# Performance work log

Hardware: AMD Instinct MI355X
Metric: run time of the kernel (lower is better)

The kernel has to match this reference:

```python
import jax, jax.numpy as jnp
import numpy as np

E = 8      # number of parts/experts
H = 128    # hidden width
D_IN = 3   # xyz coords
D_OUT = 1  # occupancy


def setup_inputs() -> dict:
    key = jax.random.key(0)
    ks = jax.random.split(key, 9)
    coords = jax.random.normal(ks[0], (1, 65536, D_IN), dtype=jnp.float32)
    s = 0.05
    return {
        "coords": coords,
        "W0": jax.random.normal(ks[1], (E, H, D_IN), dtype=jnp.float32) * s,
        "b0": jax.random.normal(ks[2], (E, H), dtype=jnp.float32) * s,
        "W1": jax.random.normal(ks[3], (E, H, H), dtype=jnp.float32) * s,
        "b1": jax.random.normal(ks[4], (E, H), dtype=jnp.float32) * s,
        "W2": jax.random.normal(ks[5], (E, H, H), dtype=jnp.float32) * s,
        "b2": jax.random.normal(ks[6], (E, H), dtype=jnp.float32) * s,
        "Wo": jax.random.normal(ks[7], (E, D_OUT, H), dtype=jnp.float32) * s,
        "bo": jax.random.normal(ks[8], (E, D_OUT), dtype=jnp.float32) * s,
    }


def reference(coords, W0, b0, W1, b1, W2, b2, Wo, bo):
    # Batched (grouped) MLP over experts: equivalent to vmap(functional_call)
    # over stacked per-part parameters in the torch module.
    # coords: [B, N, 3]; weights: [E, out, in]
    h = jax.nn.relu(jnp.einsum('bnd,ehd->ebnh', coords, W0) + b0[:, None, None, :])
    h = jax.nn.relu(jnp.einsum('ebnh,egh->ebng', h, W1) + b1[:, None, None, :])
    h = jax.nn.relu(jnp.einsum('ebnh,egh->ebng', h, W2) + b2[:, None, None, :])
    expert_out = jnp.einsum('ebnh,eoh->ebno', h, Wo) + bo[:, None, None, :]  # [E,B,N,1]
    max_occ = jnp.max(expert_out, axis=0)  # combine experts via max, [B,N,1]
    return max_occ
```

## Files before the change

kernel.cpp:

```cpp
#include <hip/hip_runtime.h>

#define NE 8
#define HD 128
#define NPTS 65536
#define TM 64

typedef __bf16 bf16x8 __attribute__((ext_vector_type(8)));
typedef __bf16 bf16x4 __attribute__((ext_vector_type(4)));
typedef float f32x4 __attribute__((ext_vector_type(4)));

__device__ __forceinline__ unsigned int f2bf(float f) {
    unsigned int u = __float_as_uint(f);
    u += 0x7FFFu + ((u >> 16) & 1u);
    return u >> 16;
}

__device__ __forceinline__ unsigned int swz(int row, int byte_in_row) {
    return (unsigned int)((row * 256 + byte_in_row) ^ ((row & 7) << 4));
}

__device__ __forceinline__ void bar_lds() {
    asm volatile("s_waitcnt lgkmcnt(0)\ns_barrier" ::: "memory");
}

template<int KB0, int KB1>
__device__ __forceinline__ void loadA128(const unsigned short* __restrict__ Ag,
                                         bf16x8 (&a)[2][4], int tc, int lr, int lg) {
#pragma unroll
    for (int ca = 0; ca < 2; ++ca)
#pragma unroll
        for (int kb = KB0; kb < KB1; ++kb)
            a[ca][kb] = *(const bf16x8*)(Ag + (tc + ca * 16 + lr) * HD + kb * 32 + lg * 8);
}

__device__ __forceinline__ void loadA32(const unsigned short* __restrict__ Ag,
                                        bf16x8 (&a)[2][1], int tc, int lr, int lg) {
#pragma unroll
    for (int ca = 0; ca < 2; ++ca)
        a[ca][0] = *(const bf16x8*)(Ag + (tc + ca * 16 + lr) * 32 + lg * 8);
}

template<int NKB, bool BSWZ, int BSTR>
__device__ __forceinline__ void gemm_core(const bf16x8 (&a)[2][NKB], const char* Bb,
                                          f32x4 (&acc)[2][4], int lr, int lg) {
#pragma unroll
    for (int kb = 0; kb < NKB; ++kb) {
        bf16x8 b[4];
#pragma unroll
        for (int nb = 0; nb < 4; ++nb) {
            int r = nb * 16 + lr;
            int byte = kb * 64 + lg * 16;
            const char* p = BSWZ ? (Bb + swz(r, byte)) : (Bb + r * BSTR + byte);
            b[nb] = *(const bf16x8*)p;
        }
#pragma unroll
        for (int ca = 0; ca < 2; ++ca)
#pragma unroll
            for (int nb = 0; nb < 4; ++nb)
                acc[ca][nb] = __builtin_amdgcn_mfma_f32_16x16x32_bf16(a[ca][kb], b[nb], acc[ca][nb], 0, 0, 0);
    }
}

__device__ __forceinline__ void epi_store(const f32x4 (&acc)[2][4], char* Db,
                                          const float* __restrict__ bias,
                                          int tc, int lr, int lg) {
#pragma unroll
    for (int ca = 0; ca < 2; ++ca) {
        int c0 = tc + ca * 16 + lg * 4;
        float4 bs = *(const float4*)(bias + c0);
#pragma unroll
        for (int nb = 0; nb < 4; ++nb) {
            int r = nb * 16 + lr;
            bf16x4 pk;
            pk[0] = (__bf16)fmaxf(acc[ca][nb][0] + bs.x, 0.f);
            pk[1] = (__bf16)fmaxf(acc[ca][nb][1] + bs.y, 0.f);
            pk[2] = (__bf16)fmaxf(acc[ca][nb][2] + bs.z, 0.f);
            pk[3] = (__bf16)fmaxf(acc[ca][nb][3] + bs.w, 0.f);
            *(bf16x4*)(Db + swz(r, c0 * 2)) = pk;
        }
    }
}

__global__ void prep_kernel(const float* __restrict__ W0,
                            const float* __restrict__ W1,
                            const float* __restrict__ W2,
                            unsigned int* __restrict__ W1b,
                            unsigned int* __restrict__ W2b,
                            unsigned int* __restrict__ W0p) {
    int i = blockIdx.x * 256 + threadIdx.x;
    float2 v = *(const float2*)(W1 + 2 * i);
    W1b[i] = f2bf(v.x) | (f2bf(v.y) << 16);
    float2 u = *(const float2*)(W2 + 2 * i);
    W2b[i] = f2bf(u.x) | (f2bf(u.y) << 16);
    if (i < NE * HD * 16) {
        int row = i >> 4;
        int kk = (i & 15) * 2;
        float a = (kk < 3) ? W0[row * 3 + kk] : 0.f;
        float b = (kk + 1 < 3) ? W0[row * 3 + kk + 1] : 0.f;
        W0p[i] = f2bf(a) | (f2bf(b) << 16);
    }
}

__global__ __launch_bounds__(256, 4) void moe_main(
    const float* __restrict__ coords,
    const float* __restrict__ b0, const float* __restrict__ b1,
    const float* __restrict__ b2,
    const float* __restrict__ Wo, const float* __restrict__ bo,
    const unsigned short* __restrict__ W0p,
    const unsigned short* __restrict__ W1b,
    const unsigned short* __restrict__ W2b,
    float* __restrict__ out) {
    __shared__ __align__(16) unsigned short hA[TM * HD];
    __shared__ __align__(16) unsigned short hB[TM * HD];
    __shared__ __align__(16) unsigned short Xp[TM * 32];
    __shared__ __align__(16) float part[256];

    const int tid = threadIdx.x;
    const int lane = tid & 63;
    const int w = tid >> 6;
    const int lr = lane & 15;
    const int lg = lane >> 4;
    const int tc = w * 32;
    const int row0 = blockIdx.x * TM;

    for (int i = tid; i < TM * 32; i += 256) Xp[i] = 0;
    __syncthreads();
    if (tid < TM * 3) {
        int r = tid / 3, k = tid % 3;
        Xp[r * 32 + k] = (unsigned short)f2bf(coords[row0 * 3 + tid]);
    }
    __syncthreads();

    float bmax = -3.0e38f;
    bf16x8 a0[2][1], a1[2][4], a2[2][4];
    loadA32(W0p, a0, tc, lr, lg);

    for (int e = 0; e < NE; ++e) {
        const unsigned short* W1e = W1b + e * HD * HD;
        const unsigned short* W2e = W2b + e * HD * HD;

        loadA128<0, 2>(W1e, a1, tc, lr, lg);
        f32x4 acc[2][4];
#pragma unroll
        for (int ca = 0; ca < 2; ++ca)
#pragma unroll
            for (int nb = 0; nb < 4; ++nb) acc[ca][nb] = (f32x4){0.f, 0.f, 0.f, 0.f};
        gemm_core<1, false, 64>(a0, (const char*)Xp, acc, lr, lg);
        epi_store(acc, (char*)hA, b0 + e * HD, tc, lr, lg);
        bar_lds();

        loadA128<2, 4>(W1e, a1, tc, lr, lg);
        loadA128<0, 2>(W2e, a2, tc, lr, lg);
#pragma unroll
        for (int ca = 0; ca < 2; ++ca)
#pragma unroll
            for (int nb = 0; nb < 4; ++nb) acc[ca][nb] = (f32x4){0.f, 0.f, 0.f, 0.f};
        gemm_core<4, true, 0>(a1, (const char*)hA, acc, lr, lg);
        epi_store(acc, (char*)hB, b1 + e * HD, tc, lr, lg);
        bar_lds();

        loadA128<2, 4>(W2e, a2, tc, lr, lg);
        loadA32(W0p + (e < 7 ? e + 1 : 7) * HD * 32, a0, tc, lr, lg);
#pragma unroll
        for (int ca = 0; ca < 2; ++ca)
#pragma unroll
            for (int nb = 0; nb < 4; ++nb) acc[ca][nb] = (f32x4){0.f, 0.f, 0.f, 0.f};
        gemm_core<4, true, 0>(a2, (const char*)hB, acc, lr, lg);

        {
            const float* b2e = b2 + e * HD;
            const float* Woe = Wo + e * HD;
            float s[4] = {0.f, 0.f, 0.f, 0.f};
#pragma unroll
            for (int ca = 0; ca < 2; ++ca) {
                int c0 = tc + ca * 16 + lg * 4;
                float4 bs = *(const float4*)(b2e + c0);
                float4 wo = *(const float4*)(Woe + c0);
#pragma unroll
                for (int nb = 0; nb < 4; ++nb) {
                    float v0 = fmaxf(acc[ca][nb][0] + bs.x, 0.f);
                    float v1 = fmaxf(acc[ca][nb][1] + bs.y, 0.f);
                    float v2 = fmaxf(acc[ca][nb][2] + bs.z, 0.f);
                    float v3 = fmaxf(acc[ca][nb][3] + bs.w, 0.f);
                    s[nb] += v0 * wo.x + v1 * wo.y + v2 * wo.z + v3 * wo.w;
                }
            }
#pragma unroll
            for (int nb = 0; nb < 4; ++nb) {
                s[nb] += __shfl_xor(s[nb], 16);
                s[nb] += __shfl_xor(s[nb], 32);
            }
            if (lg == 0) {
#pragma unroll
                for (int nb = 0; nb < 4; ++nb) part[w * 64 + nb * 16 + lr] = s[nb];
            }
        }
        bar_lds();

        if (tid < TM) {
            float v = part[tid] + part[64 + tid] + part[128 + tid] + part[192 + tid] + bo[e];
            bmax = fmaxf(bmax, v);
        }
    }

    if (tid < TM) out[row0 + tid] = bmax;
}

extern "C" void kernel_launch(void* const* d_in, const int* in_sizes, int n_in,
                              void* d_out, int out_size, void* d_ws, size_t ws_size,
                              hipStream_t stream) {
    const float* coords = (const float*)d_in[0];
    const float* W0 = (const float*)d_in[1];
    const float* b0 = (const float*)d_in[2];
    const float* W1 = (const float*)d_in[3];
    const float* b1 = (const float*)d_in[4];
    const float* W2 = (const float*)d_in[5];
    const float* b2 = (const float*)d_in[6];
    const float* Wo = (const float*)d_in[7];
    const float* bo = (const float*)d_in[8];
    float* out = (float*)d_out;

    char* ws = (char*)d_ws;
    unsigned short* W1b = (unsigned short*)(ws);
    unsigned short* W2b = (unsigned short*)(ws + 262144);
    unsigned short* W0p = (unsigned short*)(ws + 524288);

    prep_kernel<<<dim3(256), dim3(256), 0, stream>>>(
        W0, W1, W2, (unsigned int*)W1b, (unsigned int*)W2b, (unsigned int*)W0p);

    moe_main<<<dim3(NPTS / TM), dim3(256), 0, stream>>>(
        coords, b0, b1, b2, Wo, bo, W0p, W1b, W2b, out);
}
```

Measured before the change: 78.35 us.

## Retile waves as 2x2 over hidden channels and points, prefetch next expert weights

Each wave now covers 64 hidden channels by 32 points instead of 32 channels by all 64 points. This halves the number of LDS B-operand reads per MFMA, and the reduction partials drop from four per point to two. Weight loads are moved so the next expert's W0 and first half of W1 are prefetched during the last GEMM and its epilogue, to hide global latency. The X tile row stride is padded to 40 to reduce bank conflicts. The cost is roughly double the per-wave weight register footprint (a1/a2 grow to 4x4 vectors), which may hurt occupancy under launch_bounds(256,4) or cause spills.

```diff
diff --git a/kernel.cpp b/kernel.cpp
--- a/kernel.cpp
+++ b/kernel.cpp
@@ -24,53 +24,32 @@
 }
 
 template<int KB0, int KB1>
-__device__ __forceinline__ void loadA128(const unsigned short* __restrict__ Ag,
-                                         bf16x8 (&a)[2][4], int tc, int lr, int lg) {
-#pragma unroll
-    for (int ca = 0; ca < 2; ++ca)
+__device__ __forceinline__ void loadW(const unsigned short* __restrict__ Ag,
+                                      bf16x8 (&a)[4][4], int tc, int lr, int lg) {
+#pragma unroll
+    for (int ca = 0; ca < 4; ++ca)
 #pragma unroll
         for (int kb = KB0; kb < KB1; ++kb)
             a[ca][kb] = *(const bf16x8*)(Ag + (tc + ca * 16 + lr) * HD + kb * 32 + lg * 8);
 }
 
-__device__ __forceinline__ void loadA32(const unsigned short* __restrict__ Ag,
-                                        bf16x8 (&a)[2][1], int tc, int lr, int lg) {
-#pragma unroll
-    for (int ca = 0; ca < 2; ++ca)
-        a[ca][0] = *(const bf16x8*)(Ag + (tc + ca * 16 + lr) * 32 + lg * 8);
-}
-
-template<int NKB, bool BSWZ, int BSTR>
-__device__ __forceinline__ void gemm_core(const bf16x8 (&a)[2][NKB], const char* Bb,
-                                          f32x4 (&acc)[2][4], int lr, int lg) {
-#pragma unroll
-    for (int kb = 0; kb < NKB; ++kb) {
-        bf16x8 b[4];
-#pragma unroll
-        for (int nb = 0; nb < 4; ++nb) {
-            int r = nb * 16 + lr;
-            int byte = kb * 64 + lg * 16;
-            const char* p = BSWZ ? (Bb + swz(r, byte)) : (Bb + r * BSTR + byte);
-            b[nb] = *(const bf16x8*)p;
-        }
-#pragma unroll
-        for (int ca = 0; ca < 2; ++ca)
-#pragma unroll
-            for (int nb = 0; nb < 4; ++nb)
-                acc[ca][nb] = __builtin_amdgcn_mfma_f32_16x16x32_bf16(a[ca][kb], b[nb], acc[ca][nb], 0, 0, 0);
-    }
-}
-
-__device__ __forceinline__ void epi_store(const f32x4 (&acc)[2][4], char* Db,
+__device__ __forceinline__ void loadW0(const unsigned short* __restrict__ Ag,
+                                       bf16x8 (&a0)[4], int tc, int lr, int lg) {
+#pragma unroll
+    for (int ca = 0; ca < 4; ++ca)
+        a0[ca] = *(const bf16x8*)(Ag + (tc + ca * 16 + lr) * 32 + lg * 8);
+}
+
+__device__ __forceinline__ void epi_store(const f32x4 (&acc)[4][2], char* Db,
                                           const float* __restrict__ bias,
-                                          int tc, int lr, int lg) {
-#pragma unroll
-    for (int ca = 0; ca < 2; ++ca) {
+                                          int tc, int pr0, int lr, int lg) {
+#pragma unroll
+    for (int ca = 0; ca < 4; ++ca) {
         int c0 = tc + ca * 16 + lg * 4;
         float4 bs = *(const float4*)(bias + c0);
 #pragma unroll
-        for (int nb = 0; nb < 4; ++nb) {
-            int r = nb * 16 + lr;
+        for (int nb = 0; nb < 2; ++nb) {
+            int r = pr0 + nb * 16 + lr;
             bf16x4 pk;
             pk[0] = (__bf16)fmaxf(acc[ca][nb][0] + bs.x, 0.f);
             pk[1] = (__bf16)fmaxf(acc[ca][nb][1] + bs.y, 0.f);
@@ -112,72 +91,109 @@
     float* __restrict__ out) {
     __shared__ __align__(16) unsigned short hA[TM * HD];
     __shared__ __align__(16) unsigned short hB[TM * HD];
-    __shared__ __align__(16) unsigned short Xp[TM * 32];
-    __shared__ __align__(16) float part[256];
+    __shared__ __align__(16) unsigned short Xp[TM * 40];
+    __shared__ __align__(16) float part[128];
 
     const int tid = threadIdx.x;
     const int lane = tid & 63;
     const int w = tid >> 6;
     const int lr = lane & 15;
     const int lg = lane >> 4;
-    const int tc = w * 32;
+    const int ch = w & 1;
+    const int pc = w >> 1;
+    const int tc = ch * 64;
+    const int pr0 = pc * 32;
     const int row0 = blockIdx.x * TM;
 
-    for (int i = tid; i < TM * 32; i += 256) Xp[i] = 0;
+    for (int i = tid; i < TM * 40; i += 256) Xp[i] = 0;
     __syncthreads();
     if (tid < TM * 3) {
         int r = tid / 3, k = tid % 3;
-        Xp[r * 32 + k] = (unsigned short)f2bf(coords[row0 * 3 + tid]);
+        Xp[r * 40 + k] = (unsigned short)f2bf(coords[row0 * 3 + tid]);
     }
     __syncthreads();
 
     float bmax = -3.0e38f;
-    bf16x8 a0[2][1], a1[2][4], a2[2][4];
-    loadA32(W0p, a0, tc, lr, lg);
+    bf16x8 a0[4], a1[4][4], a2[4][4];
+    loadW0(W0p, a0, tc, lr, lg);
+    loadW<0, 2>(W1b, a1, tc, lr, lg);
 
     for (int e = 0; e < NE; ++e) {
         const unsigned short* W1e = W1b + e * HD * HD;
         const unsigned short* W2e = W2b + e * HD * HD;
-
-        loadA128<0, 2>(W1e, a1, tc, lr, lg);
-        f32x4 acc[2][4];
-#pragma unroll
-        for (int ca = 0; ca < 2; ++ca)
-#pragma unroll
-            for (int nb = 0; nb < 4; ++nb) acc[ca][nb] = (f32x4){0.f, 0.f, 0.f, 0.f};
-        gemm_core<1, false, 64>(a0, (const char*)Xp, acc, lr, lg);
-        epi_store(acc, (char*)hA, b0 + e * HD, tc, lr, lg);
+        const int e1 = (e < NE - 1) ? e + 1 : e;
+        f32x4 acc[4][2];
+
+#pragma unroll
+        for (int ca = 0; ca < 4; ++ca)
+#pragma unroll
+            for (int nb = 0; nb < 2; ++nb) acc[ca][nb] = (f32x4){0.f, 0.f, 0.f, 0.f};
+        {
+            bf16x8 b[2];
+#pragma unroll
+            for (int nb = 0; nb < 2; ++nb)
+                b[nb] = *(const bf16x8*)(Xp + (pr0 + nb * 16 + lr) * 40 + lg * 8);
+#pragma unroll
+            for (int ca = 0; ca < 4; ++ca)
+#pragma unroll
+                for (int nb = 0; nb < 2; ++nb)
+                    acc[ca][nb] = __builtin_amdgcn_mfma_f32_16x16x32_bf16(a0[ca], b[nb], acc[ca][nb], 0, 0, 0);
+        }
+        loadW<2, 4>(W1e, a1, tc, lr, lg);
+        epi_store(acc, (char*)hA, b0 + e * HD, tc, pr0, lr, lg);
         bar_lds();
 
-        loadA128<2, 4>(W1e, a1, tc, lr, lg);
-        loadA128<0, 2>(W2e, a2, tc, lr, lg);
-#pragma unroll
-        for (int ca = 0; ca < 2; ++ca)
-#pragma unroll
-            for (int nb = 0; nb < 4; ++nb) acc[ca][nb] = (f32x4){0.f, 0.f, 0.f, 0.f};
-        gemm_core<4, true, 0>(a1, (const char*)hA, acc, lr, lg);
-        epi_store(acc, (char*)hB, b1 + e * HD, tc, lr, lg);
+#pragma unroll
+        for (int ca = 0; ca < 4; ++ca)
+#pragma unroll
+            for (int nb = 0; nb < 2; ++nb) acc[ca][nb] = (f32x4){0.f, 0.f, 0.f, 0.f};
+#pragma unroll
+        for (int kb = 0; kb < 4; ++kb) {
+            bf16x8 b[2];
+#pragma unroll
+            for (int nb = 0; nb < 2; ++nb)
+                b[nb] = *(const bf16x8*)(((const char*)hA) + swz(pr0 + nb * 16 + lr, kb * 64 + lg * 16));
+#pragma unroll
+            for (int ca = 0; ca < 4; ++ca)
+#pragma unroll
+                for (int nb = 0; nb < 2; ++nb)
+                    acc[ca][nb] = __builtin_amdgcn_mfma_f32_16x16x32_bf16(a1[ca][kb], b[nb], acc[ca][nb], 0, 0, 0);
+        }
+        loadW<0, 2>(W2e, a2, tc, lr, lg);
+        epi_store(acc, (char*)hB, b1 + e * HD, tc, pr0, lr, lg);
         bar_lds();
 
-        loadA128<2, 4>(W2e, a2, tc, lr, lg);
-        loadA32(W0p + (e < 7 ? e + 1 : 7) * HD * 32, a0, tc, lr, lg);
-#pragma unroll
-        for (int ca = 0; ca < 2; ++ca)
-#pragma unroll
-            for (int nb = 0; nb < 4; ++nb) acc[ca][nb] = (f32x4){0.f, 0.f, 0.f, 0.f};
-        gemm_core<4, true, 0>(a2, (const char*)hB, acc, lr, lg);
+        loadW<2, 4>(W2e, a2, tc, lr, lg);
+#pragma unroll
+        for (int ca = 0; ca < 4; ++ca)
+#pragma unroll
+            for (int nb = 0; nb < 2; ++nb) acc[ca][nb] = (f32x4){0.f, 0.f, 0.f, 0.f};
+#pragma unroll
+        for (int kb = 0; kb < 4; ++kb) {
+            bf16x8 b[2];
+#pragma unroll
+            for (int nb = 0; nb < 2; ++nb)
+                b[nb] = *(const bf16x8*)(((const char*)hB) + swz(pr0 + nb * 16 + lr, kb * 64 + lg * 16));
+#pragma unroll
+            for (int ca = 0; ca < 4; ++ca)
+#pragma unroll
+                for (int nb = 0; nb < 2; ++nb)
+                    acc[ca][nb] = __builtin_amdgcn_mfma_f32_16x16x32_bf16(a2[ca][kb], b[nb], acc[ca][nb], 0, 0, 0);
+        }
+        loadW0(W0p + e1 * HD * 32, a0, tc, lr, lg);
+        loadW<0, 2>(W1b + e1 * HD * HD, a1, tc, lr, lg);
 
         {
             const float* b2e = b2 + e * HD;
             const float* Woe = Wo + e * HD;
-            float s[4] = {0.f, 0.f, 0.f, 0.f};
-#pragma unroll
-            for (int ca = 0; ca < 2; ++ca) {
+            float s[2] = {0.f, 0.f};
+#pragma unroll
+            for (int ca = 0; ca < 4; ++ca) {
                 int c0 = tc + ca * 16 + lg * 4;
                 float4 bs = *(const float4*)(b2e + c0);
                 float4 wo = *(const float4*)(Woe + c0);
 #pragma unroll
-                for (int nb = 0; nb < 4; ++nb) {
+                for (int nb = 0; nb < 2; ++nb) {
                     float v0 = fmaxf(acc[ca][nb][0] + bs.x, 0.f);
                     float v1 = fmaxf(acc[ca][nb][1] + bs.y, 0.f);
                     float v2 = fmaxf(acc[ca][nb][2] + bs.z, 0.f);
@@ -186,21 +202,18 @@
                 }
             }
 #pragma unroll
-            for (int nb = 0; nb < 4; ++nb) {
+            for (int nb = 0; nb < 2; ++nb) {
                 s[nb] += __shfl_xor(s[nb], 16);
                 s[nb] += __shfl_xor(s[nb], 32);
             }
             if (lg == 0) {
 #pragma unroll
-                for (int nb = 0; nb < 4; ++nb) part[w * 64 + nb * 16 + lr] = s[nb];
+                for (int nb = 0; nb < 2; ++nb) part[ch * 64 + pr0 + nb * 16 + lr] = s[nb];
             }
         }
         bar_lds();
 
-        if (tid < TM) {
-            float v = part[tid] + part[64 + tid] + part[128 + tid] + part[192 + tid] + bo[e];
-            bmax = fmaxf(bmax, v);
-        }
+        if (tid < TM) bmax = fmaxf(bmax, part[tid] + part[64 + tid] + bo[e]);
     }
 
     if (tid < TM) out[row0 + tid] = bmax;
```

Result: slower. 152.7 us (+94.9%).

## Drop per-expert barrier via LDS atomics and prefetch next expert weights

Applied to the files above, without the earlier changes.

The per-expert partial sums now go into an 8-slot LDS buffer through atomic adds, so the final barrier and max reduction run once after the loop instead of once per expert. Global weight loads for the next stage and next expert are issued after the current MFMA block rather than before it, which lets the loads overlap compute. The coordinate tile setup is merged into a single barrier with a padded row stride of 40. In exchange, LDS atomics add contention and make the float sums order-dependent, and more weight registers stay live at once.

```diff
diff --git a/kernel.cpp b/kernel.cpp
--- a/kernel.cpp
+++ b/kernel.cpp
@@ -101,6 +101,8 @@
     }
 }
 
+#define XPS 40
+
 __global__ __launch_bounds__(256, 4) void moe_main(
     const float* __restrict__ coords,
     const float* __restrict__ b0, const float* __restrict__ b1,
@@ -112,8 +114,8 @@
     float* __restrict__ out) {
     __shared__ __align__(16) unsigned short hA[TM * HD];
     __shared__ __align__(16) unsigned short hB[TM * HD];
-    __shared__ __align__(16) unsigned short Xp[TM * 32];
-    __shared__ __align__(16) float part[256];
+    __shared__ __align__(16) unsigned short Xp[TM * XPS];
+    __shared__ __align__(16) float part[NE * TM];
 
     const int tid = threadIdx.x;
     const int lane = tid & 63;
@@ -123,49 +125,56 @@
     const int tc = w * 32;
     const int row0 = blockIdx.x * TM;
 
-    for (int i = tid; i < TM * 32; i += 256) Xp[i] = 0;
-    __syncthreads();
-    if (tid < TM * 3) {
-        int r = tid / 3, k = tid % 3;
-        Xp[r * 32 + k] = (unsigned short)f2bf(coords[row0 * 3 + tid]);
-    }
-    __syncthreads();
-
-    float bmax = -3.0e38f;
+    if (tid < TM) {
+        unsigned int* rowp = (unsigned int*)(Xp + tid * XPS);
+        float c0 = coords[(row0 + tid) * 3 + 0];
+        float c1 = coords[(row0 + tid) * 3 + 1];
+        float c2 = coords[(row0 + tid) * 3 + 2];
+        rowp[0] = f2bf(c0) | (f2bf(c1) << 16);
+        rowp[1] = f2bf(c2);
+#pragma unroll
+        for (int i = 2; i < XPS / 2; ++i) rowp[i] = 0;
+    } else if (tid >= 128) {
+        ((float4*)part)[tid - 128] = (float4){0.f, 0.f, 0.f, 0.f};
+    }
+    bar_lds();
+
     bf16x8 a0[2][1], a1[2][4], a2[2][4];
     loadA32(W0p, a0, tc, lr, lg);
+    loadA128<0, 2>(W1b, a1, tc, lr, lg);
 
     for (int e = 0; e < NE; ++e) {
         const unsigned short* W1e = W1b + e * HD * HD;
         const unsigned short* W2e = W2b + e * HD * HD;
-
-        loadA128<0, 2>(W1e, a1, tc, lr, lg);
+        const int e1 = (e < NE - 1) ? e + 1 : e;
         f32x4 acc[2][4];
+
 #pragma unroll
         for (int ca = 0; ca < 2; ++ca)
 #pragma unroll
             for (int nb = 0; nb < 4; ++nb) acc[ca][nb] = (f32x4){0.f, 0.f, 0.f, 0.f};
-        gemm_core<1, false, 64>(a0, (const char*)Xp, acc, lr, lg);
+        gemm_core<1, false, XPS * 2>(a0, (const char*)Xp, acc, lr, lg);
+        loadA128<2, 4>(W1e, a1, tc, lr, lg);
         epi_store(acc, (char*)hA, b0 + e * HD, tc, lr, lg);
         bar_lds();
 
-        loadA128<2, 4>(W1e, a1, tc, lr, lg);
-        loadA128<0, 2>(W2e, a2, tc, lr, lg);
 #pragma unroll
         for (int ca = 0; ca < 2; ++ca)
 #pragma unroll
             for (int nb = 0; nb < 4; ++nb) acc[ca][nb] = (f32x4){0.f, 0.f, 0.f, 0.f};
         gemm_core<4, true, 0>(a1, (const char*)hA, acc, lr, lg);
+        loadA128<0, 2>(W2e, a2, tc, lr, lg);
         epi_store(acc, (char*)hB, b1 + e * HD, tc, lr, lg);
         bar_lds();
 
         loadA128<2, 4>(W2e, a2, tc, lr, lg);
-        loadA32(W0p + (e < 7 ? e + 1 : 7) * HD * 32, a0, tc, lr, lg);
 #pragma unroll
         for (int ca = 0; ca < 2; ++ca)
 #pragma unroll
             for (int nb = 0; nb < 4; ++nb) acc[ca][nb] = (f32x4){0.f, 0.f, 0.f, 0.f};
         gemm_core<4, true, 0>(a2, (const char*)hB, acc, lr, lg);
+        loadA32(W0p + e1 * HD * 32, a0, tc, lr, lg);
+        loadA128<0, 2>(W1b + e1 * HD * HD, a1, tc, lr, lg);
 
         {
             const float* b2e = b2 + e * HD;
@@ -192,18 +201,19 @@
             }
             if (lg == 0) {
 #pragma unroll
-                for (int nb = 0; nb < 4; ++nb) part[w * 64 + nb * 16 + lr] = s[nb];
+                for (int nb = 0; nb < 4; ++nb)
+                    atomicAdd(&part[e * TM + nb * 16 + lr], s[nb]);
             }
         }
-        bar_lds();
-
-        if (tid < TM) {
-            float v = part[tid] + part[64 + tid] + part[128 + tid] + part[192 + tid] + bo[e];
-            bmax = fmaxf(bmax, v);
-        }
-    }
-
-    if (tid < TM) out[row0 + tid] = bmax;
+    }
+
+    bar_lds();
+    if (tid < TM) {
+        float m = -3.0e38f;
+#pragma unroll
+        for (int e = 0; e < NE; ++e) m = fmaxf(m, part[e * TM + tid] + bo[e]);
+        out[row0 + tid] = m;
+    }
 }
 
 extern "C" void kernel_launch(void* const* d_in, const int* in_sizes, int n_in,
```

Result: slower. 83.94 us (+7.1%).
